# Kernel tuning notes

Measured on AMD Instinct MI355X. Metric: run time of the kernel, lower is better.

## Reference

```python
import jax, jax.numpy as jnp
import numpy as np

INPUT_SIZE, HIDDEN, LEVELS = 64, 256, 2
T, B = 2048, 128


def _lstm_layer(x_seq, h0, c0, W_ih, W_hh, b_ih, b_hh):
    """Run one LSTM layer over the full sequence. x_seq: [T,B,D] -> hs: [T,B,H].
    PyTorch gate order: i, f, g, o."""
    def step(carry, x_t):
        h, c = carry
        z = x_t @ W_ih.T + b_ih + h @ W_hh.T + b_hh  # [B, 4H]
        i, f, g, o = jnp.split(z, 4, axis=-1)
        i = jax.nn.sigmoid(i)
        f = jax.nn.sigmoid(f)
        g = jnp.tanh(g)
        o = jax.nn.sigmoid(o)
        c = f * c + i * g
        h = o * jnp.tanh(c)
        return (h, c), h
    _, hs = jax.lax.scan(step, (h0, c0), x_seq)
    return hs


def setup_inputs() -> dict:
    key = jax.random.key(0)
    ks = jax.random.split(key, 16)
    s = 1.0 / np.sqrt(HIDDEN)
    inp = {
        "x": jax.random.normal(ks[0], (T, B, INPUT_SIZE), dtype=jnp.float32),
        "h0": jax.random.uniform(ks[1], (LEVELS, B, HIDDEN), dtype=jnp.float32),
        "c0": jax.random.uniform(ks[2], (LEVELS, B, HIDDEN), dtype=jnp.float32),
        # layer 0 (input -> hidden)
        "W_ih0": jax.random.uniform(ks[3], (4 * HIDDEN, INPUT_SIZE), jnp.float32, -s, s),
        "W_hh0": jax.random.uniform(ks[4], (4 * HIDDEN, HIDDEN), jnp.float32, -s, s),
        "b_ih0": jax.random.uniform(ks[5], (4 * HIDDEN,), jnp.float32, -s, s),
        "b_hh0": jax.random.uniform(ks[6], (4 * HIDDEN,), jnp.float32, -s, s),
        # layer 1 (hidden -> hidden)
        "W_ih1": jax.random.uniform(ks[7], (4 * HIDDEN, HIDDEN), jnp.float32, -s, s),
        "W_hh1": jax.random.uniform(ks[8], (4 * HIDDEN, HIDDEN), jnp.float32, -s, s),
        "b_ih1": jax.random.uniform(ks[9], (4 * HIDDEN,), jnp.float32, -s, s),
        "b_hh1": jax.random.uniform(ks[10], (4 * HIDDEN,), jnp.float32, -s, s),
        # linear head hidden -> 1
        "W_lin": jax.random.uniform(ks[11], (1, HIDDEN), jnp.float32, -s, s),
        "b_lin": jax.random.uniform(ks[12], (1,), jnp.float32, -s, s),
    }
    return inp


def reference(x, h0, c0, W_ih0, W_hh0, b_ih0, b_hh0, W_ih1, W_hh1, b_ih1, b_hh1, W_lin, b_lin):
    hs0 = _lstm_layer(x, h0[0], c0[0], W_ih0, W_hh0, b_ih0, b_hh0)   # [T,B,H]
    hs1 = _lstm_layer(hs0, h0[1], c0[1], W_ih1, W_hh1, b_ih1, b_hh1)  # [T,B,H]
    out = hs1 @ W_lin.T + b_lin  # [T,B,1]
    return out[..., 0]  # [T,B] (matches torch stack().squeeze())
```

## Files before the change

kernel.cpp:

```cpp
#include <hip/hip_runtime.h>

constexpr int TT   = 2048;
constexpr int NB   = 128;
constexpr int NI   = 64;
constexpr int NH   = 256;
constexpr int NGRP = 128;
constexpr int NWG  = 256;
constexpr int NTHR = 512;
constexpr int R0   = 8;
constexpr int R1   = 16;
constexpr int HLAG = 8;
constexpr int SLOT = (NH / 2) * NB;

__device__ unsigned g_c[64];
__device__ unsigned g_cnt = 0, g_gen = 0;

__device__ __forceinline__ float sigm(float v) { return 1.0f / (1.0f + __expf(-v)); }
__device__ __forceinline__ float tanhfast(float v) {
    float e = __expf(2.0f * v);
    return 1.0f - 2.0f / (e + 1.0f);
}
__device__ __forceinline__ float asfl(unsigned u) { return __uint_as_float(u); }
__device__ __forceinline__ unsigned f2bf(float f) {
    unsigned u = __float_as_uint(f);
    return (u + 0x7fffu + ((u >> 16) & 1u)) >> 16;
}

__device__ __forceinline__ unsigned long long ldq(const unsigned* p) {
    return __hip_atomic_load((const unsigned long long*)p, __ATOMIC_RELAXED,
                             __HIP_MEMORY_SCOPE_AGENT);
}
__device__ __forceinline__ unsigned ldd(const unsigned* p) {
    return __hip_atomic_load(p, __ATOMIC_RELAXED, __HIP_MEMORY_SCOPE_AGENT);
}
__device__ __forceinline__ void std_(unsigned* p, unsigned v) {
    __hip_atomic_store(p, v, __ATOMIC_RELAXED, __HIP_MEMORY_SCOPE_AGENT);
}
__device__ __forceinline__ void bump(unsigned* p) {
    (void)__hip_atomic_fetch_add(p, 1u, __ATOMIC_RELAXED, __HIP_MEMORY_SCOPE_AGENT);
}

__device__ __forceinline__ void pollboth(unsigned n0, unsigned n1, int lane) {
    const unsigned* p = &g_c[(lane & 1) * 32];
    for (;;) {
        unsigned v = ldd(p);
        unsigned c0v = (unsigned)__shfl((int)v, 0);
        unsigned c1v = (unsigned)__shfl((int)v, 1);
        if (c0v >= n0 && c1v >= n1) return;
        __builtin_amdgcn_s_sleep(1);
    }
}

__device__ __forceinline__ void gridbar(unsigned k, bool last) {
    __syncthreads();
    if (threadIdx.x == 0) {
        __threadfence();
        unsigned a = __hip_atomic_fetch_add(&g_cnt, 1u, __ATOMIC_ACQ_REL,
                                            __HIP_MEMORY_SCOPE_AGENT);
        if (a == k * NWG - 1u) {
            if (last) {
                __hip_atomic_store(&g_cnt, 0u, __ATOMIC_RELAXED, __HIP_MEMORY_SCOPE_AGENT);
                __hip_atomic_store(&g_gen, 0u, __ATOMIC_RELEASE, __HIP_MEMORY_SCOPE_AGENT);
            } else {
                __hip_atomic_store(&g_gen, k, __ATOMIC_RELEASE, __HIP_MEMORY_SCOPE_AGENT);
            }
        } else if (!last) {
            while (__hip_atomic_load(&g_gen, __ATOMIC_RELAXED,
                                     __HIP_MEMORY_SCOPE_AGENT) < k)
                __builtin_amdgcn_s_sleep(1);
        }
        __threadfence();
    }
    __syncthreads();
}

#define STEPQ(Q, HA, HB)                                   \
    acc[0]  += w00.Q * (HA); acc[1]  += w00.Q * (HB);      \
    acc[2]  += w01.Q * (HA); acc[3]  += w01.Q * (HB);      \
    acc[4]  += w02.Q * (HA); acc[5]  += w02.Q * (HB);      \
    acc[6]  += w03.Q * (HA); acc[7]  += w03.Q * (HB);      \
    acc[8]  += w10.Q * (HA); acc[9]  += w10.Q * (HB);      \
    acc[10] += w11.Q * (HA); acc[11] += w11.Q * (HB);      \
    acc[12] += w12.Q * (HA); acc[13] += w12.Q * (HB);      \
    acc[14] += w13.Q * (HA); acc[15] += w13.Q * (HB);

#define LOADW(W, K, kk)                                                        \
    float4 w00 = *(const float4*)((W) + (size_t)(0 * NH + j0    ) * (K) + (kk)); \
    float4 w01 = *(const float4*)((W) + (size_t)(1 * NH + j0    ) * (K) + (kk)); \
    float4 w02 = *(const float4*)((W) + (size_t)(2 * NH + j0    ) * (K) + (kk)); \
    float4 w03 = *(const float4*)((W) + (size_t)(3 * NH + j0    ) * (K) + (kk)); \
    float4 w10 = *(const float4*)((W) + (size_t)(0 * NH + j0 + 1) * (K) + (kk)); \
    float4 w11 = *(const float4*)((W) + (size_t)(1 * NH + j0 + 1) * (K) + (kk)); \
    float4 w12 = *(const float4*)((W) + (size_t)(2 * NH + j0 + 1) * (K) + (kk)); \
    float4 w13 = *(const float4*)((W) + (size_t)(3 * NH + j0 + 1) * (K) + (kk));

__device__ __forceinline__ void partH_bf(const float* __restrict__ W, int j0,
                                         int kbase,
                                         const unsigned* __restrict__ hd,
                                         int lane, float* acc) {
    const unsigned* hp = hd + (size_t)(kbase >> 1) * NB + (lane << 1);
    #pragma unroll 4
    for (int i = 0; i < 16; ++i) {
        const int kk = kbase + (i << 2);
        LOADW(W, NH, kk)
        unsigned long long q0 = ldq(hp + (size_t)(2 * i) * NB);
        unsigned long long q1 = ldq(hp + (size_t)(2 * i + 1) * NB);
        unsigned d00 = (unsigned)q0, d01 = (unsigned)(q0 >> 32);
        unsigned d10 = (unsigned)q1, d11 = (unsigned)(q1 >> 32);
        STEPQ(x, asfl(d00 << 16),          asfl(d01 << 16))
        STEPQ(y, asfl(d00 & 0xffff0000u),  asfl(d01 & 0xffff0000u))
        STEPQ(z, asfl(d10 << 16),          asfl(d11 << 16))
        STEPQ(w, asfl(d10 & 0xffff0000u),  asfl(d11 & 0xffff0000u))
    }
}

__device__ __forceinline__ void partX(const float* __restrict__ W, int j0,
                                      int k0, const float* __restrict__ xp,
                                      int lane, float* acc) {
    #pragma unroll
    for (int i4 = 0; i4 < 4; ++i4) {
        const int kk = k0 + (i4 << 2);
        LOADW(W, NI, kk)
        float4 xa = *(const float4*)(xp + (size_t)(lane << 1) * NI + kk);
        float4 xb = *(const float4*)(xp + (size_t)((lane << 1) + 1) * NI + kk);
        STEPQ(x, xa.x, xb.x)
        STEPQ(y, xa.y, xb.y)
        STEPQ(z, xa.z, xb.z)
        STEPQ(w, xa.w, xb.w)
    }
}

__global__ void __launch_bounds__(NTHR, 2) lstm2(
    const float* __restrict__ x,
    const float* __restrict__ h0in, const float* __restrict__ c0in,
    const float* __restrict__ Wih0, const float* __restrict__ Whh0,
    const float* __restrict__ bih0, const float* __restrict__ bhh0,
    const float* __restrict__ Wih1, const float* __restrict__ Whh1,
    const float* __restrict__ bih1, const float* __restrict__ bhh1,
    const float* __restrict__ Wlin, const float* __restrict__ blin,
    float* __restrict__ out,
    unsigned* __restrict__ h0d, unsigned* __restrict__ h1d)
{
    __shared__ __align__(16) float4 zp4[16 * NB];
    __shared__ float red[4];
    __shared__ unsigned go_w;

    const int tid  = threadIdx.x;
    const int gid  = blockIdx.x;
    const bool is1 = gid >= NGRP;
    const int g    = is1 ? gid - NGRP : gid;
    const int j0   = g * 2;
    const int lane = tid & 63;
    const int wv   = __builtin_amdgcn_readfirstlane(tid >> 6);

    unsigned* ownc   = is1 ? &g_c[32] : &g_c[0];

    float4 bsA = make_float4(0, 0, 0, 0), bsB = bsA;
    float cA = 0.f, cB = 0.f;
    if (tid < 128) {
        const float* bi = is1 ? bih1 : bih0;
        const float* bh = is1 ? bhh1 : bhh0;
        bsA.x = bi[0 * NH + j0] + bh[0 * NH + j0];
        bsA.y = bi[1 * NH + j0] + bh[1 * NH + j0];
        bsA.z = bi[2 * NH + j0] + bh[2 * NH + j0];
        bsA.w = bi[3 * NH + j0] + bh[3 * NH + j0];
        bsB.x = bi[0 * NH + j0 + 1] + bh[0 * NH + j0 + 1];
        bsB.y = bi[1 * NH + j0 + 1] + bh[1 * NH + j0 + 1];
        bsB.z = bi[2 * NH + j0 + 1] + bh[2 * NH + j0 + 1];
        bsB.w = bi[3 * NH + j0 + 1] + bh[3 * NH + j0 + 1];
        const float* cbase = c0in + (is1 ? 1 : 0) * NB * NH + (size_t)tid * NH + j0;
        cA = cbase[0]; cB = cbase[1];
        const float* hbase = h0in + (is1 ? 1 : 0) * NB * NH + (size_t)tid * NH + j0;
        unsigned d = (f2bf(hbase[1]) << 16) | f2bf(hbase[0]);
        unsigned* hT = is1 ? h1d : h0d;
        const int islot = is1 ? (R1 - 1) : (R0 - 1);
        std_(hT + (size_t)islot * SLOT + (size_t)g * NB + tid, d);
    }
    if (tid == 0) go_w = 0;
    const float blv = blin[0];
    asm volatile("s_waitcnt vmcnt(0)" ::: "memory");
    __syncthreads();
    if (tid == 0) bump(ownc);

    if (!is1) {
        for (int s = 0; s < TT + HLAG; ++s) {
            const unsigned tgt = (unsigned)(s + 1);
            unsigned need0 = (s < TT) ? 128u * (unsigned)(s + 1) : 0u;
            unsigned need1 = (s >= R0) ? 128u * (unsigned)(s - R0 + 2) : 0u;
            if (wv == 0) {
                pollboth(need0, need1, lane);
                if (lane == 0)
                    __hip_atomic_store(&go_w, tgt, __ATOMIC_RELAXED,
                                       __HIP_MEMORY_SCOPE_WORKGROUP);
            } else {
                while (__hip_atomic_load(&go_w, __ATOMIC_RELAXED,
                                         __HIP_MEMORY_SCOPE_WORKGROUP) < tgt) {}
            }

            if (s < TT) {
                float acc[16] = {0,0,0,0,0,0,0,0,0,0,0,0,0,0,0,0};
                if (wv < 4)
                    partH_bf(Whh0, j0, wv * 64,
                             h0d + (size_t)((s + R0 - 1) & (R0 - 1)) * SLOT, lane, acc);
                else
                    partX(Wih0, j0, (wv - 4) * 16, x + (size_t)s * NB * NI, lane, acc);
                const int base0 = ((wv << 1) + 0) * NB + (lane << 1);
                const int base1 = ((wv << 1) + 1) * NB + (lane << 1);
                zp4[base0]     = make_float4(acc[0],  acc[2],  acc[4],  acc[6]);
                zp4[base0 + 1] = make_float4(acc[1],  acc[3],  acc[5],  acc[7]);
                zp4[base1]     = make_float4(acc[8],  acc[10], acc[12], acc[14]);
                zp4[base1 + 1] = make_float4(acc[9],  acc[11], acc[13], acc[15]);
            }
            if (s >= HLAG && tid >= 256) {
                const int u = s - HLAG;
                const int k = tid - 256;
                unsigned d = ldd(h1d + (size_t)(u & (R1 - 1)) * SLOT
                                 + (size_t)(k >> 1) * NB + g);
                float hv = (k & 1) ? asfl(d & 0xffff0000u) : asfl(d << 16);
                float p = Wlin[k] * hv;
                #pragma unroll
                for (int off = 32; off; off >>= 1) p += __shfl_down(p, off);
                if (lane == 0) red[wv - 4] = p;
            }
            __syncthreads();

            if (s < TT && tid < 128) {
                float4 zA = bsA, zB = bsB;
                #pragma unroll
                for (int q = 0; q < 8; ++q) {
                    float4 a = zp4[(q * 2 + 0) * NB + tid];
                    float4 b = zp4[(q * 2 + 1) * NB + tid];
                    zA.x += a.x; zA.y += a.y; zA.z += a.z; zA.w += a.w;
                    zB.x += b.x; zB.y += b.y; zB.z += b.z; zB.w += b.w;
                }
                float iA = sigm(zA.x), fA = sigm(zA.y), gA = tanhfast(zA.z), oA = sigm(zA.w);
                cA = fA * cA + iA * gA;
                float hA = oA * tanhfast(cA);
                float iB = sigm(zB.x), fB = sigm(zB.y), gB = tanhfast(zB.z), oB = sigm(zB.w);
                cB = fB * cB + iB * gB;
                float hB = oB * tanhfast(cB);
                unsigned d = (f2bf(hB) << 16) | f2bf(hA);
                std_(h0d + (size_t)(s & (R0 - 1)) * SLOT + (size_t)g * NB + tid, d);
            }
            if (s >= HLAG && tid == 256)
                out[(size_t)(s - HLAG) * NB + g] = red[0] + red[1] + red[2] + red[3] + blv;

            asm volatile("s_waitcnt vmcnt(0)" ::: "memory");
            __syncthreads();
            if (s < TT && tid == 0) bump(&g_c[0]);
        }
    } else {
        for (int t = 0; t < TT; ++t) {
            const unsigned tgt = (unsigned)(t + 1);
            unsigned need0 = 128u * (unsigned)(t + 2);
            unsigned need1 = 128u * (unsigned)(t + 1);
            if (wv == 0) {
                pollboth(need0, need1, lane);
                if (lane == 0)
                    __hip_atomic_store(&go_w, tgt, __ATOMIC_RELAXED,
                                       __HIP_MEMORY_SCOPE_WORKGROUP);
            } else {
                while (__hip_atomic_load(&go_w, __ATOMIC_RELAXED,
                                         __HIP_MEMORY_SCOPE_WORKGROUP) < tgt) {}
            }

            float acc[16] = {0,0,0,0,0,0,0,0,0,0,0,0,0,0,0,0};
            if (wv < 4)
                partH_bf(Wih1, j0, wv * 64,
                         h0d + (size_t)(t & (R0 - 1)) * SLOT, lane, acc);
            else
                partH_bf(Whh1, j0, (wv - 4) * 64,
                         h1d + (size_t)((t + R1 - 1) & (R1 - 1)) * SLOT, lane, acc);
            const int base0 = ((wv << 1) + 0) * NB + (lane << 1);
            const int base1 = ((wv << 1) + 1) * NB + (lane << 1);
            zp4[base0]     = make_float4(acc[0],  acc[2],  acc[4],  acc[6]);
            zp4[base0 + 1] = make_float4(acc[1],  acc[3],  acc[5],  acc[7]);
            zp4[base1]     = make_float4(acc[8],  acc[10], acc[12], acc[14]);
            zp4[base1 + 1] = make_float4(acc[9],  acc[11], acc[13], acc[15]);
            __syncthreads();

            if (tid < 128) {
                float4 zA = bsA, zB = bsB;
                #pragma unroll
                for (int q = 0; q < 8; ++q) {
                    float4 a = zp4[(q * 2 + 0) * NB + tid];
                    float4 b = zp4[(q * 2 + 1) * NB + tid];
                    zA.x += a.x; zA.y += a.y; zA.z += a.z; zA.w += a.w;
                    zB.x += b.x; zB.y += b.y; zB.z += b.z; zB.w += b.w;
                }
                float iA = sigm(zA.x), fA = sigm(zA.y), gA = tanhfast(zA.z), oA = sigm(zA.w);
                cA = fA * cA + iA * gA;
                float hA = oA * tanhfast(cA);
                float iB = sigm(zB.x), fB = sigm(zB.y), gB = tanhfast(zB.z), oB = sigm(zB.w);
                cB = fB * cB + iB * gB;
                float hB = oB * tanhfast(cB);
                unsigned d = (f2bf(hB) << 16) | f2bf(hA);
                std_(h1d + (size_t)(t & (R1 - 1)) * SLOT + (size_t)g * NB + tid, d);
            }
            asm volatile("s_waitcnt vmcnt(0)" ::: "memory");
            __syncthreads();
            if (tid == 0) bump(&g_c[32]);
        }
    }

    gridbar(1, false);
    if (gid == 0 && tid == 0) {
        __hip_atomic_store(&g_c[0],  0u, __ATOMIC_RELAXED, __HIP_MEMORY_SCOPE_AGENT);
        __hip_atomic_store(&g_c[32], 0u, __ATOMIC_RELAXED, __HIP_MEMORY_SCOPE_AGENT);
    }
    gridbar(2, true);
}

extern "C" void kernel_launch(void* const* d_in, const int* in_sizes, int n_in,
                              void* d_out, int out_size, void* d_ws, size_t ws_size,
                              hipStream_t stream)
{
    const float* x    = (const float*)d_in[0];
    const float* h0in = (const float*)d_in[1];
    const float* c0in = (const float*)d_in[2];
    const float* Wih0 = (const float*)d_in[3];
    const float* Whh0 = (const float*)d_in[4];
    const float* bih0 = (const float*)d_in[5];
    const float* bhh0 = (const float*)d_in[6];
    const float* Wih1 = (const float*)d_in[7];
    const float* Whh1 = (const float*)d_in[8];
    const float* bih1 = (const float*)d_in[9];
    const float* bhh1 = (const float*)d_in[10];
    const float* Wlin = (const float*)d_in[11];
    const float* blin = (const float*)d_in[12];
    float* out = (float*)d_out;

    unsigned* h0d = (unsigned*)d_ws;
    unsigned* h1d = h0d + (size_t)R0 * SLOT;

    void* args[] = { &x, &h0in, &c0in, &Wih0, &Whh0, &bih0, &bhh0,
                     &Wih1, &Whh1, &bih1, &bhh1, &Wlin, &blin,
                     &out, &h0d, &h1d };
    hipLaunchCooperativeKernel((void*)lstm2, dim3(NWG), dim3(NTHR), args, 0, stream);
}
```

Before: 22.43 ms.

## Split recurrent and input projections, precompute off critical path, shard counters

Each step's work is split into a critical recurrent part (Whh·h, now spread over all 8 waves with 32-wide K slices) and a non-critical input projection (Wih·x or Wih1·h0). The input projection for the next step is computed into a second LDS buffer right after publishing h, so it runs off the dependency chain. The single progress counter per layer is replaced by 8 cache-line-sharded counters polled in parallel by 8 lanes, which cuts atomic contention. This adds an extra wait and barrier per step and more LDS use, which could reduce occupancy.

```diff
diff --git a/kernel.cpp b/kernel.cpp
--- a/kernel.cpp
+++ b/kernel.cpp
@@ -1,18 +1,18 @@
 #include <hip/hip_runtime.h>
 
-constexpr int TT   = 2048;
-constexpr int NB   = 128;
-constexpr int NI   = 64;
-constexpr int NH   = 256;
+constexpr int TT = 2048;
+constexpr int NB = 128;
+constexpr int NI = 64;
+constexpr int NH = 256;
 constexpr int NGRP = 128;
 constexpr int NWG  = 256;
 constexpr int NTHR = 512;
-constexpr int R0   = 8;
-constexpr int R1   = 16;
-constexpr int HLAG = 8;
+constexpr int R0 = 8;
+constexpr int R1 = 16;
 constexpr int SLOT = (NH / 2) * NB;
 
-__device__ unsigned g_c[64];
+__device__ unsigned g_cA[8 * 32];
+__device__ unsigned g_cB[8 * 32];
 __device__ unsigned g_cnt = 0, g_gen = 0;
 
 __device__ __forceinline__ float sigm(float v) { return 1.0f / (1.0f + __expf(-v)); }
@@ -40,14 +40,26 @@
     (void)__hip_atomic_fetch_add(p, 1u, __ATOMIC_RELAXED, __HIP_MEMORY_SCOPE_AGENT);
 }
 
-__device__ __forceinline__ void pollboth(unsigned n0, unsigned n1, int lane) {
-    const unsigned* p = &g_c[(lane & 1) * 32];
+__device__ __forceinline__ void pollc(const unsigned* base, unsigned tgt, int lane) {
     for (;;) {
-        unsigned v = ldd(p);
-        unsigned c0v = (unsigned)__shfl((int)v, 0);
-        unsigned c1v = (unsigned)__shfl((int)v, 1);
-        if (c0v >= n0 && c1v >= n1) return;
+        unsigned v = tgt;
+        if (lane < 8) v = ldd(base + lane * 32);
+        if (__all((int)(v >= tgt))) return;
         __builtin_amdgcn_s_sleep(1);
+    }
+}
+
+__device__ __forceinline__ void wg_wait(const unsigned* shards, unsigned ctgt,
+                                        unsigned* go, unsigned gtgt,
+                                        int wv, int lane) {
+    if (wv == 0) {
+        pollc(shards, ctgt, lane);
+        if (lane == 0)
+            __hip_atomic_store(go, gtgt, __ATOMIC_RELAXED, __HIP_MEMORY_SCOPE_WORKGROUP);
+    } else {
+        while (__hip_atomic_load(go, __ATOMIC_RELAXED,
+                                 __HIP_MEMORY_SCOPE_WORKGROUP) < gtgt)
+            __builtin_amdgcn_s_sleep(1);
     }
 }
 
@@ -94,13 +106,12 @@
     float4 w12 = *(const float4*)((W) + (size_t)(2 * NH + j0 + 1) * (K) + (kk)); \
     float4 w13 = *(const float4*)((W) + (size_t)(3 * NH + j0 + 1) * (K) + (kk));
 
-__device__ __forceinline__ void partH_bf(const float* __restrict__ W, int j0,
-                                         int kbase,
-                                         const unsigned* __restrict__ hd,
-                                         int lane, float* acc) {
+__device__ __forceinline__ void partH32(const float* __restrict__ W, int j0,
+                                        int kbase, const unsigned* __restrict__ hd,
+                                        int lane, float* acc) {
     const unsigned* hp = hd + (size_t)(kbase >> 1) * NB + (lane << 1);
-    #pragma unroll 4
-    for (int i = 0; i < 16; ++i) {
+    #pragma unroll
+    for (int i = 0; i < 8; ++i) {
         const int kk = kbase + (i << 2);
         LOADW(W, NH, kk)
         unsigned long long q0 = ldq(hp + (size_t)(2 * i) * NB);
@@ -114,11 +125,11 @@
     }
 }
 
-__device__ __forceinline__ void partX(const float* __restrict__ W, int j0,
-                                      int k0, const float* __restrict__ xp,
-                                      int lane, float* acc) {
+__device__ __forceinline__ void partX8(const float* __restrict__ W, int j0,
+                                       int k0, const float* __restrict__ xp,
+                                       int lane, float* acc) {
     #pragma unroll
-    for (int i4 = 0; i4 < 4; ++i4) {
+    for (int i4 = 0; i4 < 2; ++i4) {
         const int kk = k0 + (i4 << 2);
         LOADW(W, NI, kk)
         float4 xa = *(const float4*)(xp + (size_t)(lane << 1) * NI + kk);
@@ -128,6 +139,16 @@
         STEPQ(z, xa.z, xb.z)
         STEPQ(w, xa.w, xb.w)
     }
+}
+
+__device__ __forceinline__ void writezp(float4* zp, int wv, int lane,
+                                        const float* acc) {
+    const int b0 = ((wv << 1) + 0) * NB + (lane << 1);
+    const int b1 = ((wv << 1) + 1) * NB + (lane << 1);
+    zp[b0]     = make_float4(acc[0],  acc[2],  acc[4],  acc[6]);
+    zp[b0 + 1] = make_float4(acc[1],  acc[3],  acc[5],  acc[7]);
+    zp[b1]     = make_float4(acc[8],  acc[10], acc[12], acc[14]);
+    zp[b1 + 1] = make_float4(acc[9],  acc[11], acc[13], acc[15]);
 }
 
 __global__ void __launch_bounds__(NTHR, 2) lstm2(
@@ -141,9 +162,10 @@
     float* __restrict__ out,
     unsigned* __restrict__ h0d, unsigned* __restrict__ h1d)
 {
-    __shared__ __align__(16) float4 zp4[16 * NB];
+    __shared__ __align__(16) float4 zpC[16 * NB];
+    __shared__ __align__(16) float4 zpS[16 * NB];
     __shared__ float red[4];
-    __shared__ unsigned go_w;
+    __shared__ unsigned goA, goB;
 
     const int tid  = threadIdx.x;
     const int gid  = blockIdx.x;
@@ -153,21 +175,23 @@
     const int lane = tid & 63;
     const int wv   = __builtin_amdgcn_readfirstlane(tid >> 6);
 
-    unsigned* ownc   = is1 ? &g_c[32] : &g_c[0];
+    unsigned* ownS = is1 ? g_cB : g_cA;
+    unsigned* crsS = is1 ? g_cA : g_cB;
+    unsigned* myline = ownS + (g & 7) * 32;
 
     float4 bsA = make_float4(0, 0, 0, 0), bsB = bsA;
     float cA = 0.f, cB = 0.f;
     if (tid < 128) {
         const float* bi = is1 ? bih1 : bih0;
         const float* bh = is1 ? bhh1 : bhh0;
-        bsA.x = bi[0 * NH + j0] + bh[0 * NH + j0];
-        bsA.y = bi[1 * NH + j0] + bh[1 * NH + j0];
-        bsA.z = bi[2 * NH + j0] + bh[2 * NH + j0];
-        bsA.w = bi[3 * NH + j0] + bh[3 * NH + j0];
-        bsB.x = bi[0 * NH + j0 + 1] + bh[0 * NH + j0 + 1];
-        bsB.y = bi[1 * NH + j0 + 1] + bh[1 * NH + j0 + 1];
-        bsB.z = bi[2 * NH + j0 + 1] + bh[2 * NH + j0 + 1];
-        bsB.w = bi[3 * NH + j0 + 1] + bh[3 * NH + j0 + 1];
+        bsA.x = bi[0*NH + j0] + bh[0*NH + j0];
+        bsA.y = bi[1*NH + j0] + bh[1*NH + j0];
+        bsA.z = bi[2*NH + j0] + bh[2*NH + j0];
+        bsA.w = bi[3*NH + j0] + bh[3*NH + j0];
+        bsB.x = bi[0*NH + j0+1] + bh[0*NH + j0+1];
+        bsB.y = bi[1*NH + j0+1] + bh[1*NH + j0+1];
+        bsB.z = bi[2*NH + j0+1] + bh[2*NH + j0+1];
+        bsB.w = bi[3*NH + j0+1] + bh[3*NH + j0+1];
         const float* cbase = c0in + (is1 ? 1 : 0) * NB * NH + (size_t)tid * NH + j0;
         cA = cbase[0]; cB = cbase[1];
         const float* hbase = h0in + (is1 ? 1 : 0) * NB * NH + (size_t)tid * NH + j0;
@@ -176,62 +200,39 @@
         const int islot = is1 ? (R1 - 1) : (R0 - 1);
         std_(hT + (size_t)islot * SLOT + (size_t)g * NB + tid, d);
     }
-    if (tid == 0) go_w = 0;
+    if (tid == 0) { goA = 0; goB = 0; }
     const float blv = blin[0];
     asm volatile("s_waitcnt vmcnt(0)" ::: "memory");
     __syncthreads();
-    if (tid == 0) bump(ownc);
+    if (tid == 0) bump(myline);
 
     if (!is1) {
-        for (int s = 0; s < TT + HLAG; ++s) {
-            const unsigned tgt = (unsigned)(s + 1);
-            unsigned need0 = (s < TT) ? 128u * (unsigned)(s + 1) : 0u;
-            unsigned need1 = (s >= R0) ? 128u * (unsigned)(s - R0 + 2) : 0u;
-            if (wv == 0) {
-                pollboth(need0, need1, lane);
-                if (lane == 0)
-                    __hip_atomic_store(&go_w, tgt, __ATOMIC_RELAXED,
-                                       __HIP_MEMORY_SCOPE_WORKGROUP);
-            } else {
-                while (__hip_atomic_load(&go_w, __ATOMIC_RELAXED,
-                                         __HIP_MEMORY_SCOPE_WORKGROUP) < tgt) {}
-            }
-
+        {
+            float acc[16] = {0,0,0,0,0,0,0,0,0,0,0,0,0,0,0,0};
+            partX8(Wih0, j0, wv * 8, x, lane, acc);
+            writezp(zpS, wv, lane, acc);
+        }
+        for (int s = 0; s < TT + 7; ++s) {
             if (s < TT) {
+                wg_wait(ownS, 16u * (unsigned)(s + 1), &goA, (unsigned)(s + 1), wv, lane);
                 float acc[16] = {0,0,0,0,0,0,0,0,0,0,0,0,0,0,0,0};
-                if (wv < 4)
-                    partH_bf(Whh0, j0, wv * 64,
-                             h0d + (size_t)((s + R0 - 1) & (R0 - 1)) * SLOT, lane, acc);
-                else
-                    partX(Wih0, j0, (wv - 4) * 16, x + (size_t)s * NB * NI, lane, acc);
-                const int base0 = ((wv << 1) + 0) * NB + (lane << 1);
-                const int base1 = ((wv << 1) + 1) * NB + (lane << 1);
-                zp4[base0]     = make_float4(acc[0],  acc[2],  acc[4],  acc[6]);
-                zp4[base0 + 1] = make_float4(acc[1],  acc[3],  acc[5],  acc[7]);
-                zp4[base1]     = make_float4(acc[8],  acc[10], acc[12], acc[14]);
-                zp4[base1 + 1] = make_float4(acc[9],  acc[11], acc[13], acc[15]);
-            }
-            if (s >= HLAG && tid >= 256) {
-                const int u = s - HLAG;
-                const int k = tid - 256;
-                unsigned d = ldd(h1d + (size_t)(u & (R1 - 1)) * SLOT
-                                 + (size_t)(k >> 1) * NB + g);
-                float hv = (k & 1) ? asfl(d & 0xffff0000u) : asfl(d << 16);
-                float p = Wlin[k] * hv;
-                #pragma unroll
-                for (int off = 32; off; off >>= 1) p += __shfl_down(p, off);
-                if (lane == 0) red[wv - 4] = p;
-            }
-            __syncthreads();
-
+                partH32(Whh0, j0, wv * 32,
+                        h0d + (size_t)((s + R0 - 1) & (R0 - 1)) * SLOT, lane, acc);
+                writezp(zpC, wv, lane, acc);
+            }
+            __syncthreads();
             if (s < TT && tid < 128) {
                 float4 zA = bsA, zB = bsB;
                 #pragma unroll
                 for (int q = 0; q < 8; ++q) {
-                    float4 a = zp4[(q * 2 + 0) * NB + tid];
-                    float4 b = zp4[(q * 2 + 1) * NB + tid];
-                    zA.x += a.x; zA.y += a.y; zA.z += a.z; zA.w += a.w;
-                    zB.x += b.x; zB.y += b.y; zB.z += b.z; zB.w += b.w;
+                    float4 a  = zpC[(q*2+0)*NB + tid];
+                    float4 b4 = zpC[(q*2+1)*NB + tid];
+                    float4 c4 = zpS[(q*2+0)*NB + tid];
+                    float4 d4 = zpS[(q*2+1)*NB + tid];
+                    zA.x += a.x + c4.x; zA.y += a.y + c4.y;
+                    zA.z += a.z + c4.z; zA.w += a.w + c4.w;
+                    zB.x += b4.x + d4.x; zB.y += b4.y + d4.y;
+                    zB.z += b4.z + d4.z; zB.w += b4.w + d4.w;
                 }
                 float iA = sigm(zA.x), fA = sigm(zA.y), gA = tanhfast(zA.z), oA = sigm(zA.w);
                 cA = fA * cA + iA * gA;
@@ -242,51 +243,58 @@
                 unsigned d = (f2bf(hB) << 16) | f2bf(hA);
                 std_(h0d + (size_t)(s & (R0 - 1)) * SLOT + (size_t)g * NB + tid, d);
             }
-            if (s >= HLAG && tid == 256)
-                out[(size_t)(s - HLAG) * NB + g] = red[0] + red[1] + red[2] + red[3] + blv;
-
             asm volatile("s_waitcnt vmcnt(0)" ::: "memory");
             __syncthreads();
-            if (s < TT && tid == 0) bump(&g_c[0]);
+            if (s < TT && tid == 0) bump(myline);
+
+            if (s >= 5)
+                wg_wait(crsS, 16u * (unsigned)(s - 5), &goB, (unsigned)(s - 4), wv, lane);
+            if (s + 1 < TT) {
+                float acc[16] = {0,0,0,0,0,0,0,0,0,0,0,0,0,0,0,0};
+                partX8(Wih0, j0, wv * 8, x + (size_t)(s + 1) * NB * NI, lane, acc);
+                writezp(zpS, wv, lane, acc);
+            }
+            if (s >= 7 && tid >= 256) {
+                const int u = s - 7;
+                const int k = tid - 256;
+                unsigned d = ldd(h1d + (size_t)(u & (R1 - 1)) * SLOT
+                                 + (size_t)(k >> 1) * NB + g);
+                float hv = (k & 1) ? asfl(d & 0xffff0000u) : asfl(d << 16);
+                float p = Wlin[k] * hv;
+                #pragma unroll
+                for (int off = 32; off; off >>= 1) p += __shfl_down(p, off);
+                if (lane == 0) red[wv - 4] = p;
+            }
+            __syncthreads();
+            if (s >= 7 && tid == 256)
+                out[(size_t)(s - 7) * NB + g] = red[0] + red[1] + red[2] + red[3] + blv;
         }
     } else {
+        wg_wait(crsS, 32u, &goB, 1u, wv, lane);
+        {
+            float acc[16] = {0,0,0,0,0,0,0,0,0,0,0,0,0,0,0,0};
+            partH32(Wih1, j0, wv * 32, h0d, lane, acc);
+            writezp(zpS, wv, lane, acc);
+        }
         for (int t = 0; t < TT; ++t) {
-            const unsigned tgt = (unsigned)(t + 1);
-            unsigned need0 = 128u * (unsigned)(t + 2);
-            unsigned need1 = 128u * (unsigned)(t + 1);
-            if (wv == 0) {
-                pollboth(need0, need1, lane);
-                if (lane == 0)
-                    __hip_atomic_store(&go_w, tgt, __ATOMIC_RELAXED,
-                                       __HIP_MEMORY_SCOPE_WORKGROUP);
-            } else {
-                while (__hip_atomic_load(&go_w, __ATOMIC_RELAXED,
-                                         __HIP_MEMORY_SCOPE_WORKGROUP) < tgt) {}
-            }
-
+            wg_wait(ownS, 16u * (unsigned)(t + 1), &goA, (unsigned)(t + 1), wv, lane);
             float acc[16] = {0,0,0,0,0,0,0,0,0,0,0,0,0,0,0,0};
-            if (wv < 4)
-                partH_bf(Wih1, j0, wv * 64,
-                         h0d + (size_t)(t & (R0 - 1)) * SLOT, lane, acc);
-            else
-                partH_bf(Whh1, j0, (wv - 4) * 64,
-                         h1d + (size_t)((t + R1 - 1) & (R1 - 1)) * SLOT, lane, acc);
-            const int base0 = ((wv << 1) + 0) * NB + (lane << 1);
-            const int base1 = ((wv << 1) + 1) * NB + (lane << 1);
-            zp4[base0]     = make_float4(acc[0],  acc[2],  acc[4],  acc[6]);
-            zp4[base0 + 1] = make_float4(acc[1],  acc[3],  acc[5],  acc[7]);
-            zp4[base1]     = make_float4(acc[8],  acc[10], acc[12], acc[14]);
-            zp4[base1 + 1] = make_float4(acc[9],  acc[11], acc[13], acc[15]);
-            __syncthreads();
-
+            partH32(Whh1, j0, wv * 32,
+                    h1d + (size_t)((t + R1 - 1) & (R1 - 1)) * SLOT, lane, acc);
+            writezp(zpC, wv, lane, acc);
+            __syncthreads();
             if (tid < 128) {
                 float4 zA = bsA, zB = bsB;
                 #pragma unroll
                 for (int q = 0; q < 8; ++q) {
-                    float4 a = zp4[(q * 2 + 0) * NB + tid];
-                    float4 b = zp4[(q * 2 + 1) * NB + tid];
-                    zA.x += a.x; zA.y += a.y; zA.z += a.z; zA.w += a.w;
-                    zB.x += b.x; zB.y += b.y; zB.z += b.z; zB.w += b.w;
+                    float4 a  = zpC[(q*2+0)*NB + tid];
+                    float4 b4 = zpC[(q*2+1)*NB + tid];
+                    float4 c4 = zpS[(q*2+0)*NB + tid];
+                    float4 d4 = zpS[(q*2+1)*NB + tid];
+                    zA.x += a.x + c4.x; zA.y += a.y + c4.y;
+                    zA.z += a.z + c4.z; zA.w += a.w + c4.w;
+                    zB.x += b4.x + d4.x; zB.y += b4.y + d4.y;
+                    zB.z += b4.z + d4.z; zB.w += b4.w + d4.w;
                 }
                 float iA = sigm(zA.x), fA = sigm(zA.y), gA = tanhfast(zA.z), oA = sigm(zA.w);
                 cA = fA * cA + iA * gA;
@@ -299,14 +307,26 @@
             }
             asm volatile("s_waitcnt vmcnt(0)" ::: "memory");
             __syncthreads();
-            if (tid == 0) bump(&g_c[32]);
+            if (tid == 0) bump(myline);
+
+            if (t + 1 < TT) {
+                wg_wait(crsS, 16u * (unsigned)(t + 3), &goB, (unsigned)(t + 2), wv, lane);
+                float acc2[16] = {0,0,0,0,0,0,0,0,0,0,0,0,0,0,0,0};
+                partH32(Wih1, j0, wv * 32,
+                        h0d + (size_t)((t + 1) & (R0 - 1)) * SLOT, lane, acc2);
+                writezp(zpS, wv, lane, acc2);
+            }
         }
     }
 
     gridbar(1, false);
-    if (gid == 0 && tid == 0) {
-        __hip_atomic_store(&g_c[0],  0u, __ATOMIC_RELAXED, __HIP_MEMORY_SCOPE_AGENT);
-        __hip_atomic_store(&g_c[32], 0u, __ATOMIC_RELAXED, __HIP_MEMORY_SCOPE_AGENT);
+    if (gid == 0) {
+        if (tid < 8)
+            __hip_atomic_store(&g_cA[tid * 32], 0u, __ATOMIC_RELAXED,
+                               __HIP_MEMORY_SCOPE_AGENT);
+        else if (tid < 16)
+            __hip_atomic_store(&g_cB[(tid - 8) * 32], 0u, __ATOMIC_RELAXED,
+                               __HIP_MEMORY_SCOPE_AGENT);
     }
     gridbar(2, true);
 }
```

After: 24.15 ms. +7.7%, slower.
